# Kernel tuning notes

Measured on AMD Instinct MI355X. Metric: run time of the kernel, lower is better.

## Reference

```python
import jax, jax.numpy as jnp
import numpy as np

SHIFT = 1  # shift_direction fixed to +1 (original picks +/-1 randomly at init)


def setup_inputs() -> dict:
    key = jax.random.key(0)
    k1, k2 = jax.random.split(key)
    x = jax.random.normal(k1, (1, 64, 56, 56), dtype=jnp.float32)
    W = jax.random.normal(k2, (64, 3, 2, 64), dtype=jnp.float32)
    return {"x": x, "W": W}


def reference(x, W):
    # permute 'ijkl -> iljk' and flatten (j,k) -> columns: (1,1,56,3584)
    t2 = jnp.transpose(x, (0, 3, 1, 2)).reshape(1, 1, 56, 3584)
    # unfold kernel (3,1), padding (1,0): three vertically shifted copies with zero pad
    pad = jnp.pad(t2, ((0, 0), (0, 0), (1, 1), (0, 0)))
    taps = jnp.stack([pad[:, 0, t:t + 56, :] for t in range(3)], axis=1)  # (1,3,56,3584)
    taps = taps.reshape(1, 3, 56, 64, 56)  # (m, tap k, o=orig-l, j=channels, n=orig-k)
    # contract taps (k=3) and channels (j=64) against weight (i,k,l,j)
    t3 = jnp.einsum('mkojn,iklj->mioln', taps, W)  # (1,64,56,2,56)
    # merge (o,l)->112, circular roll, split back, sum over the pair dim
    t4 = t3.reshape(1, 64, 112, 56)
    t4 = jnp.roll(t4, SHIFT, axis=2)
    t4 = t4.reshape(1, 64, 56, 2, 56).sum(axis=3)  # (1,64,56,56)
    # final circular roll along last spatial axis
    return jnp.roll(t4, SHIFT, axis=3)
```

## Files before the change

kernel.cpp:

```cpp
#include <hip/hip_runtime.h>

#define SP 56
#define CH 64
#define XSTRIDE 3136

__global__ void tsc_prep(const float* __restrict__ W, float4* __restrict__ Cv) {
  int t = blockIdx.x * blockDim.x + threadIdx.x;
  if (t >= CH * CH) return;
  int i = t & 63;
  int j = t >> 6;
  const float* Wi = W + i * 384 + j;
  float w00 = Wi[0];
  float w01 = Wi[64];
  float w10 = Wi[128];
  float w11 = Wi[192];
  float w20 = Wi[256];
  float w21 = Wi[320];
  Cv[j * 64 + i]        = make_float4(w01, w00 + w11, w10 + w21, w20);
  Cv[4096 + j * 64 + i] = make_float4(w10, w20, w01, w11);
}

__global__ __launch_bounds__(64) void tsc_main(const float* __restrict__ x,
                                               const float4* __restrict__ Cv,
                                               float* __restrict__ out) {
  const int i  = threadIdx.x;
  const int og = blockIdx.x;
  const int n  = blockIdx.y;
  const int o0 = og * 4;
  const int ns = (n + SP - 1) % SP;
  const float* xb = x + ns * SP;
  const float4* cb = Cv + i;

  float acc0 = 0.f, acc1 = 0.f, acc2 = 0.f, acc3 = 0.f;

  if (og >= 1 && og <= 12) {
    const float* xw = xb + (o0 - 2);
#pragma unroll 4
    for (int j = 0; j < CH; ++j) {
      const float4 c = cb[j * 64];
      const float* xj = xw + j * XSTRIDE;
      float w0 = xj[0], w1 = xj[1], w2 = xj[2], w3 = xj[3];
      float w4 = xj[4], w5 = xj[5], w6 = xj[6];
      acc0 += c.x * w0 + c.y * w1 + c.z * w2 + c.w * w3;
      acc1 += c.x * w1 + c.y * w2 + c.z * w3 + c.w * w4;
      acc2 += c.x * w2 + c.y * w3 + c.z * w4 + c.w * w5;
      acc3 += c.x * w3 + c.y * w4 + c.z * w5 + c.w * w6;
    }
  } else if (og == 13) {
    const float* xw = xb + 50;
#pragma unroll 4
    for (int j = 0; j < CH; ++j) {
      const float4 c = cb[j * 64];
      const float* xj = xw + j * XSTRIDE;
      float w0 = xj[0], w1 = xj[1], w2 = xj[2];
      float w3 = xj[3], w4 = xj[4], w5 = xj[5];
      acc0 += c.x * w0 + c.y * w1 + c.z * w2 + c.w * w3;
      acc1 += c.x * w1 + c.y * w2 + c.z * w3 + c.w * w4;
      acc2 += c.x * w2 + c.y * w3 + c.z * w4 + c.w * w5;
      acc3 += c.x * w3 + c.y * w4 + c.z * w5;
    }
  } else {
    float accD = 0.f;
#pragma unroll 4
    for (int j = 0; j < CH; ++j) {
      const float4 c = cb[j * 64];
      const float4 d = cb[4096 + j * 64];
      const float* xj = xb + j * XSTRIDE;
      float w2 = xj[0], w3 = xj[1], w4 = xj[2], w5 = xj[3], w6 = xj[4];
      acc1 += c.y * w2 + c.z * w3 + c.w * w4;
      acc2 += c.x * w2 + c.y * w3 + c.z * w4 + c.w * w5;
      acc3 += c.x * w3 + c.y * w4 + c.z * w5 + c.w * w6;
      accD += d.x * xj[0] + d.y * xj[1] + d.z * xj[54] + d.w * xj[55];
    }
    acc0 = accD;
  }

  float* ob = out + i * XSTRIDE + o0 * SP + n;
  ob[0]       = acc0;
  ob[SP]      = acc1;
  ob[2 * SP]  = acc2;
  ob[3 * SP]  = acc3;
}

extern "C" void kernel_launch(void* const* d_in, const int* in_sizes, int n_in,
                              void* d_out, int out_size, void* d_ws, size_t ws_size,
                              hipStream_t stream) {
  const float* x = (const float*)d_in[0];
  const float* W = (const float*)d_in[1];
  float* out = (float*)d_out;
  float4* Cv = (float4*)d_ws;

  tsc_prep<<<dim3(16), dim3(256), 0, stream>>>(W, Cv);
  tsc_main<<<dim3(14, 56), dim3(64), 0, stream>>>(x, Cv, out);
}
```

Before: 71.77 us.

## Split channel reduction across four waves with LDS-staged input window

The main kernel now uses 256 threads per block: the 8-wide input window for all 64 channels is staged once into shared memory, including wraparound and zero padding, so the per-thread global loads and three-way branching go away. Each of the four waves handles 16 input channels, and partial sums are combined through a shared-memory reduction before the stores. This gives four times the threads per block and shorter serial loops, which should hide latency better, at the cost of two barriers and extra LDS traffic.

```diff
diff --git a/kernel.cpp b/kernel.cpp
--- a/kernel.cpp
+++ b/kernel.cpp
@@ -20,66 +20,75 @@
   Cv[4096 + j * 64 + i] = make_float4(w10, w20, w01, w11);
 }
 
-__global__ __launch_bounds__(64) void tsc_main(const float* __restrict__ x,
-                                               const float4* __restrict__ Cv,
-                                               float* __restrict__ out) {
-  const int i  = threadIdx.x;
+__global__ __launch_bounds__(256) void tsc_main(const float* __restrict__ x,
+                                                const float4* __restrict__ Cv,
+                                                float* __restrict__ out) {
+  __shared__ float xs[CH][8];
+  __shared__ float red[4][4][64];
+
+  const int t  = threadIdx.x;
+  const int i  = t & 63;
+  const int w  = t >> 6;
   const int og = blockIdx.x;
   const int n  = blockIdx.y;
   const int o0 = og * 4;
   const int ns = (n + SP - 1) % SP;
-  const float* xb = x + ns * SP;
+
+  const float* xrow = x + ns * SP;
+#pragma unroll
+  for (int u = t; u < CH * 8; u += 256) {
+    int j = u >> 3;
+    int b = u & 7;
+    int g = o0 - 2 + b;
+    if (g < 0) g += SP;
+    float v = (g < SP) ? xrow[j * XSTRIDE + g] : 0.f;
+    xs[j][b] = v;
+  }
+  __syncthreads();
+
+  float a0 = 0.f, a1 = 0.f, a2 = 0.f, a3 = 0.f;
   const float4* cb = Cv + i;
+  const int j0 = w * 16;
 
-  float acc0 = 0.f, acc1 = 0.f, acc2 = 0.f, acc3 = 0.f;
-
-  if (og >= 1 && og <= 12) {
-    const float* xw = xb + (o0 - 2);
+  if (og != 0) {
 #pragma unroll 4
-    for (int j = 0; j < CH; ++j) {
-      const float4 c = cb[j * 64];
-      const float* xj = xw + j * XSTRIDE;
-      float w0 = xj[0], w1 = xj[1], w2 = xj[2], w3 = xj[3];
-      float w4 = xj[4], w5 = xj[5], w6 = xj[6];
-      acc0 += c.x * w0 + c.y * w1 + c.z * w2 + c.w * w3;
-      acc1 += c.x * w1 + c.y * w2 + c.z * w3 + c.w * w4;
-      acc2 += c.x * w2 + c.y * w3 + c.z * w4 + c.w * w5;
-      acc3 += c.x * w3 + c.y * w4 + c.z * w5 + c.w * w6;
-    }
-  } else if (og == 13) {
-    const float* xw = xb + 50;
-#pragma unroll 4
-    for (int j = 0; j < CH; ++j) {
-      const float4 c = cb[j * 64];
-      const float* xj = xw + j * XSTRIDE;
-      float w0 = xj[0], w1 = xj[1], w2 = xj[2];
-      float w3 = xj[3], w4 = xj[4], w5 = xj[5];
-      acc0 += c.x * w0 + c.y * w1 + c.z * w2 + c.w * w3;
-      acc1 += c.x * w1 + c.y * w2 + c.z * w3 + c.w * w4;
-      acc2 += c.x * w2 + c.y * w3 + c.z * w4 + c.w * w5;
-      acc3 += c.x * w3 + c.y * w4 + c.z * w5;
+    for (int jj = 0; jj < 16; ++jj) {
+      int j = j0 + jj;
+      float4 c = cb[j * 64];
+      float x0 = xs[j][0], x1 = xs[j][1], x2 = xs[j][2], x3 = xs[j][3];
+      float x4 = xs[j][4], x5 = xs[j][5], x6 = xs[j][6];
+      a0 += c.x * x0 + c.y * x1 + c.z * x2 + c.w * x3;
+      a1 += c.x * x1 + c.y * x2 + c.z * x3 + c.w * x4;
+      a2 += c.x * x2 + c.y * x3 + c.z * x4 + c.w * x5;
+      a3 += c.x * x3 + c.y * x4 + c.z * x5 + c.w * x6;
     }
   } else {
-    float accD = 0.f;
 #pragma unroll 4
-    for (int j = 0; j < CH; ++j) {
-      const float4 c = cb[j * 64];
-      const float4 d = cb[4096 + j * 64];
-      const float* xj = xb + j * XSTRIDE;
-      float w2 = xj[0], w3 = xj[1], w4 = xj[2], w5 = xj[3], w6 = xj[4];
-      acc1 += c.y * w2 + c.z * w3 + c.w * w4;
-      acc2 += c.x * w2 + c.y * w3 + c.z * w4 + c.w * w5;
-      acc3 += c.x * w3 + c.y * w4 + c.z * w5 + c.w * w6;
-      accD += d.x * xj[0] + d.y * xj[1] + d.z * xj[54] + d.w * xj[55];
+    for (int jj = 0; jj < 16; ++jj) {
+      int j = j0 + jj;
+      float4 c = cb[j * 64];
+      float4 d = cb[4096 + j * 64];
+      float x0 = xs[j][0], x1 = xs[j][1], x2 = xs[j][2], x3 = xs[j][3];
+      float x4 = xs[j][4], x5 = xs[j][5], x6 = xs[j][6];
+      a0 += d.x * x2 + d.y * x3 + d.z * x0 + d.w * x1;
+      a1 += c.y * x2 + c.z * x3 + c.w * x4;
+      a2 += c.x * x2 + c.y * x3 + c.z * x4 + c.w * x5;
+      a3 += c.x * x3 + c.y * x4 + c.z * x5 + c.w * x6;
     }
-    acc0 = accD;
   }
 
-  float* ob = out + i * XSTRIDE + o0 * SP + n;
-  ob[0]       = acc0;
-  ob[SP]      = acc1;
-  ob[2 * SP]  = acc2;
-  ob[3 * SP]  = acc3;
+  red[w][0][i] = a0;
+  red[w][1][i] = a1;
+  red[w][2][i] = a2;
+  red[w][3][i] = a3;
+  __syncthreads();
+
+  {
+    int s  = t >> 6;
+    int ii = t & 63;
+    float v = red[0][s][ii] + red[1][s][ii] + red[2][s][ii] + red[3][s][ii];
+    out[ii * XSTRIDE + (o0 + s) * SP + n] = v;
+  }
 }
 
 extern "C" void kernel_launch(void* const* d_in, const int* in_sizes, int n_in,
@@ -91,5 +100,5 @@
   float4* Cv = (float4*)d_ws;
 
   tsc_prep<<<dim3(16), dim3(256), 0, stream>>>(W, Cv);
-  tsc_main<<<dim3(14, 56), dim3(64), 0, stream>>>(x, Cv, out);
+  tsc_main<<<dim3(14, 56), dim3(256), 0, stream>>>(x, Cv, out);
 }
```

Measured after the change: 64.83 us. 9.7% less time.
